# Kernel optimization log

Measured on AMD Instinct MI355X. Metric: run time of the kernel, lower is better.

Reference implementation:

```python
import jax, jax.numpy as jnp
import numpy as np

N_E = 8192
E_DIM = 256
BETA = 0.25


def setup_inputs() -> dict:
    key = jax.random.key(0)
    k1, k2 = jax.random.split(key)
    z = jax.random.normal(k1, (16, E_DIM, 32, 32), dtype=jnp.float32)
    # nn.Embedding init: uniform(-1/n_e, 1/n_e)
    e_w = jax.random.uniform(k2, (N_E, E_DIM), dtype=jnp.float32,
                             minval=-1.0 / N_E, maxval=1.0 / N_E)
    return {"z": z, "e_w": e_w}


def reference(z, e_w):
    B, C, H, W = z.shape  # C == e_dim
    n_e = e_w.shape[0]
    # (B,C,H,W) -> (N, D)
    z_flat = jnp.transpose(z, (0, 2, 3, 1)).reshape(-1, C)
    # squared euclidean distances: ||z||^2 + ||e||^2 - 2 z.e  -> (N, n_e)
    z_sq = jnp.sum(z_flat * z_flat, axis=1, keepdims=True)
    e_sq = jnp.sum(e_w * e_w, axis=1)
    distances = z_sq + e_sq[None, :] - 2.0 * (z_flat @ e_w.T)
    indices = jnp.argmin(distances, axis=1)  # (N,)
    one_hot = jax.nn.one_hot(indices, n_e, dtype=z.dtype)  # (N, n_e)
    # one_hot @ e_w == gather
    z_q_flat = e_w[indices]
    z_q = jnp.transpose(z_q_flat.reshape(B, H, W, C), (0, 3, 1, 2))
    sg = jax.lax.stop_gradient
    loss_embed = jnp.mean((sg(z_q) - z) ** 2)
    loss_commit = jnp.mean((z_q - sg(z)) ** 2)
    loss = loss_embed + BETA * loss_commit
    # straight-through estimator
    z_q_st = z + sg(z_q - z)
    avg_probs = jnp.mean(one_hot, axis=0)
    perplexity = jnp.exp(-jnp.sum(avg_probs * jnp.log(avg_probs + 1e-10)))
    return loss, z_q_st, perplexity, one_hot, indices
```

## Files before the change

kernel.cpp:

```cpp
#include <hip/hip_runtime.h>
#include <hip/hip_bf16.h>
#include <math.h>

#define N_ROWS 16384
#define DIM    256
#define NE     8192
#define QMARGIN 21

#define SOFF 4194308

typedef __bf16 bf16x8 __attribute__((ext_vector_type(8)));
typedef float  f32x4  __attribute__((ext_vector_type(4)));
typedef float  vf4    __attribute__((ext_vector_type(4)));

__device__ __forceinline__ void gload_lds16(const __bf16* g, __bf16* l) {
  __builtin_amdgcn_global_load_lds(
      (const __attribute__((address_space(1))) unsigned int*)g,
      (__attribute__((address_space(3))) unsigned int*)l, 16, 0, 0);
}

__global__ void k_prep(const float* __restrict__ z, float* __restrict__ zf,
                       __bf16* __restrict__ zfb) {
  __shared__ float tile[32][33];
  int ct = blockIdx.x, ht = blockIdx.y, b = blockIdx.z;
  int tx = threadIdx.x & 31, ty = threadIdx.x >> 5;
  int c0 = ct * 32, hw0 = ht * 32;
  const size_t zb = (size_t)b * 256 * 1024;
#pragma unroll
  for (int p = 0; p < 4; ++p) {
    int c = p * 8 + ty;
    tile[c][tx] = z[zb + (size_t)(c0 + c) * 1024 + hw0 + tx];
  }
  __syncthreads();
#pragma unroll
  for (int p = 0; p < 4; ++p) {
    int r = p * 8 + ty;
    zf[(size_t)(b * 1024 + hw0 + r) * DIM + c0 + tx] = tile[tx][r];
  }
  if (threadIdx.x < 128) {
    int r = threadIdx.x >> 2, kc = threadIdx.x & 3;
    int row = b * 1024 + hw0 + r;
    bf16x8 v;
#pragma unroll
    for (int j = 0; j < 8; ++j) v[j] = (__bf16)tile[kc * 8 + j][r];
    int tn = row >> 7, g = (row >> 4) & 7, m15 = row & 15, kt = c0 >> 5;
    *(bf16x8*)(zfb + (size_t)tn * 32768 + kt * 4096 + g * 512 + (kc * 16 + m15) * 8) = v;
  }
}

__global__ void k_cvt_e(const float* __restrict__ ew, __bf16* __restrict__ ewb) {
  int gid = blockIdx.x * 256 + threadIdx.x;
  int r = gid >> 5, kc8 = gid & 31;
  const float* s = ew + (size_t)r * DIM + kc8 * 8;
  float4 v0 = *(const float4*)s, v1 = *(const float4*)(s + 4);
  bf16x8 v = {(__bf16)v0.x, (__bf16)v0.y, (__bf16)v0.z, (__bf16)v0.w,
              (__bf16)v1.x, (__bf16)v1.y, (__bf16)v1.z, (__bf16)v1.w};
  int t = r >> 7, g = (r >> 4) & 7, m15 = r & 15, kt = kc8 >> 2, kc = kc8 & 3;
  *(bf16x8*)(ewb + (size_t)t * 32768 + kt * 4096 + g * 512 + (kc * 16 + m15) * 8) = v;
}

__global__ __launch_bounds__(256, 2) void k_score(const __bf16* __restrict__ zfb,
                                                  const __bf16* __restrict__ ewb,
                                                  int2* __restrict__ part2) {
  __shared__ __align__(16) __bf16 Afull[32768];
  __shared__ __align__(16) __bf16 Bs[2][4096];
  const int tid = threadIdx.x;
  const int lane = tid & 63, wave = tid >> 6;
  const int wm = wave >> 1, wn = wave & 1;
  const int quad = lane >> 4, l15 = lane & 15;
  const int bx = blockIdx.x, byc = blockIdx.y;
  const __bf16* Ag = zfb + (size_t)bx * 32768;
  const __bf16* Bg = ewb + (size_t)byc * 262144;

  {
    const int base = wave * 8192;
#pragma unroll
    for (int i = 0; i < 16; ++i)
      gload_lds16(Ag + base + i * 512 + lane * 8, Afull + base + i * 512);
  }
  {
    const int boff = wave * 1024;
    gload_lds16(Bg + boff + lane * 8, Bs[0] + boff);
    gload_lds16(Bg + boff + 512 + lane * 8, Bs[0] + boff + 512);
  }

  f32x4 acc[4][4];
#pragma unroll
  for (int i = 0; i < 4; ++i)
#pragma unroll
    for (int j = 0; j < 4; ++j) acc[i][j] = (f32x4){0.f, 0.f, 0.f, 0.f};
  int r1[16], r2[16];
#pragma unroll
  for (int i = 0; i < 16; ++i) { r1[i] = 0x7fffffff; r2[i] = 0x7fffffff; }

  for (int it = 0; it < 64; ++it) {
    const int bt = it >> 3, kt = it & 7, buf = it & 1;
    __syncthreads();
    if (it < 63) {
      const int nx = it + 1;
      const __bf16* src = Bg + (nx >> 3) * 32768 + (nx & 7) * 4096 + wave * 1024;
      gload_lds16(src + lane * 8, Bs[buf ^ 1] + wave * 1024);
      gload_lds16(src + 512 + lane * 8, Bs[buf ^ 1] + wave * 1024 + 512);
    }
    bf16x8 af[4], bfr[4];
#pragma unroll
    for (int mi = 0; mi < 4; ++mi)
      af[mi] = *(const bf16x8*)(Afull + kt * 4096 + (wm * 4 + mi) * 512 + lane * 8);
#pragma unroll
    for (int ni = 0; ni < 4; ++ni)
      bfr[ni] = *(const bf16x8*)(Bs[buf] + (wn * 4 + ni) * 512 + lane * 8);
#pragma unroll
    for (int mi = 0; mi < 4; ++mi)
#pragma unroll
      for (int ni = 0; ni < 4; ++ni)
        acc[mi][ni] = __builtin_amdgcn_mfma_f32_16x16x32_bf16(af[mi], bfr[ni],
                                                              acc[mi][ni], 0, 0, 0);
    if (kt == 7) {
      const int colb = byc * 1024 + bt * 128 + wn * 64;
#pragma unroll
      for (int mi = 0; mi < 4; ++mi) {
#pragma unroll
        for (int rg = 0; rg < 4; ++rg) {
          const int idx = mi * 4 + rg;
          float s0 = -2.f * acc[mi][0][rg], s1 = -2.f * acc[mi][1][rg];
          float s2 = -2.f * acc[mi][2][rg], s3 = -2.f * acc[mi][3][rg];
          int q0 = min(max((int)((s0 + 1.0f) * 131072.0f), 0), 262143);
          int q1 = min(max((int)((s1 + 1.0f) * 131072.0f), 0), 262143);
          int q2 = min(max((int)((s2 + 1.0f) * 131072.0f), 0), 262143);
          int q3 = min(max((int)((s3 + 1.0f) * 131072.0f), 0), 262143);
          int k0 = (q0 << 13) | (colb + l15);
          int k1 = (q1 << 13) | (colb + 16 + l15);
          int k2 = (q2 << 13) | (colb + 32 + l15);
          int k3 = (q3 << 13) | (colb + 48 + l15);
          int a = min(k0, k1), bb = max(k0, k1);
          int c = min(k2, k3), dd = max(k2, k3);
          int t1 = min(a, c);
          int t2 = min(max(a, c), min(bb, dd));
          int n1 = min(r1[idx], t1);
          int n2 = min(max(r1[idx], t1), min(r2[idx], t2));
          r1[idx] = n1; r2[idx] = n2;
        }
      }
#pragma unroll
      for (int i = 0; i < 4; ++i)
#pragma unroll
        for (int j = 0; j < 4; ++j) acc[i][j] = (f32x4){0.f, 0.f, 0.f, 0.f};
    }
  }

#pragma unroll
  for (int mi = 0; mi < 4; ++mi) {
#pragma unroll
    for (int rg = 0; rg < 4; ++rg) {
      const int idx = mi * 4 + rg;
      int k1 = r1[idx], k2 = r2[idx];
#pragma unroll
      for (int d = 1; d < 16; d <<= 1) {
        int o1 = __shfl_xor(k1, d), o2 = __shfl_xor(k2, d);
        k2 = min(max(k1, o1), min(k2, o2));
        k1 = min(k1, o1);
      }
      if (l15 == 0) {
        int row = bx * 128 + wm * 64 + mi * 16 + quad * 4 + rg;
        int2 v; v.x = k1; v.y = k2;
        part2[row * 16 + byc * 2 + wn] = v;
      }
    }
  }
}

__device__ __forceinline__ float np_sumsq_128(const float* __restrict__ p) {
  float r[8];
#pragma unroll
  for (int j = 0; j < 8; ++j) r[j] = __fmul_rn(p[j], p[j]);
  for (int i = 8; i < 128; i += 8) {
#pragma unroll
    for (int j = 0; j < 8; ++j) r[j] = __fadd_rn(r[j], __fmul_rn(p[i + j], p[i + j]));
  }
  return __fadd_rn(__fadd_rn(__fadd_rn(r[0], r[1]), __fadd_rn(r[2], r[3])),
                   __fadd_rn(__fadd_rn(r[4], r[5]), __fadd_rn(r[6], r[7])));
}

__global__ __launch_bounds__(256) void k_pick(const int2* __restrict__ part2,
                                              const float* __restrict__ zf,
                                              const float* __restrict__ ew,
                                              float* __restrict__ idxF,
                                              float* __restrict__ losspart) {
  __shared__ int cand[4][40];
  __shared__ int cnts[4];
  const int t = threadIdx.x, lane = t & 63, wv = t >> 6;
  const int row = blockIdx.x * 4 + wv;
  if (lane == 0) cnts[wv] = 0;
  int2 pv;
  if (lane < 16) pv = part2[row * 16 + lane];
  else { pv.x = 0x7fffffff; pv.y = 0x7fffffff; }
  int kmin = pv.x;
#pragma unroll
  for (int d = 1; d < 64; d <<= 1) kmin = min(kmin, __shfl_xor(kmin, d));
  const int qthr = min((kmin >> 13) + QMARGIN, 262143);
  const int kthr = (qthr << 13) | 8191;
  __syncthreads();
  if (lane < 16) {
    if (pv.x <= kthr) { int p = atomicAdd(&cnts[wv], 1); cand[wv][p] = pv.x & 8191; }
    if (pv.y <= kthr) { int p = atomicAdd(&cnts[wv], 1); cand[wv][p] = pv.y & 8191; }
  }
  __syncthreads();
  const int cnt = cnts[wv];
  const float* zr = zf + (size_t)row * DIM;
  float bd = INFINITY; int bj = 0x7fffffff;
  if (lane < cnt) {
    int j = cand[wv][lane];
    const float* e = ew + (size_t)j * DIM;
    float acc = 0.f;
    for (int k = 0; k < DIM; ++k) acc = __builtin_fmaf(zr[k], e[k], acc);
    float esq = __fadd_rn(np_sumsq_128(e), np_sumsq_128(e + 128));
    float zsq = __fadd_rn(np_sumsq_128(zr), np_sumsq_128(zr + 128));
    bd = __fsub_rn(__fadd_rn(zsq, esq), __fmul_rn(2.0f, acc));
    bj = j;
  }
#pragma unroll
  for (int d = 1; d < 64; d <<= 1) {
    float od = __shfl_xor(bd, d); int oj = __shfl_xor(bj, d);
    if (od < bd || (od == bd && oj < bj)) { bd = od; bj = oj; }
  }
  int c = lane * 4;
  float4 e4 = *reinterpret_cast<const float4*>(ew + (size_t)bj * DIM + c);
  float4 z4 = *reinterpret_cast<const float4*>(zr + c);
  float t0 = __fsub_rn(e4.x, z4.x), t1 = __fsub_rn(e4.y, z4.y);
  float t2 = __fsub_rn(e4.z, z4.z), t3 = __fsub_rn(e4.w, z4.w);
  float s = __fadd_rn(__fadd_rn(__fmul_rn(t0, t0), __fmul_rn(t1, t1)),
                      __fadd_rn(__fmul_rn(t2, t2), __fmul_rn(t3, t3)));
#pragma unroll
  for (int d = 1; d < 64; d <<= 1) s += __shfl_xor(s, d);
  if (lane == 0) {
    idxF[row] = (float)bj;
    losspart[row] = s;
  }
}

__global__ __launch_bounds__(256) void k_scalars(const float* __restrict__ idxF,
                                                 const float* __restrict__ losspart,
                                                 float* __restrict__ out) {
  __shared__ int hist[NE];
  __shared__ float red[256];
  int t = threadIdx.x;
  for (int i = t; i < NE; i += 256) hist[i] = 0;
  __syncthreads();
  float ls = 0.f;
  for (int i = t; i < N_ROWS; i += 256) {
    atomicAdd(&hist[(int)idxF[i]], 1);
    ls += losspart[i];
  }
  __syncthreads();
  float es = 0.f;
  for (int i = t; i < NE; i += 256) {
    float p = (float)hist[i] * (1.0f / 16384.0f);
    es += p * logf(p + 1e-10f);
  }
  red[t] = es; __syncthreads();
  for (int w = 128; w > 0; w >>= 1) { if (t < w) red[t] += red[t + w]; __syncthreads(); }
  float esum = red[0]; __syncthreads();
  red[t] = ls; __syncthreads();
  for (int w = 128; w > 0; w >>= 1) { if (t < w) red[t] += red[t + w]; __syncthreads(); }
  if (t == 0) {
    out[4194305] = expf(-esum);
    float m = red[0] * (1.0f / 4194304.0f);
    out[0] = __fadd_rn(m, __fmul_rn(0.25f, m));
  }
}

__global__ void k_zq_out(const float* __restrict__ z, const float* __restrict__ ew,
                         const float* __restrict__ idxF, float* __restrict__ out) {
  __shared__ float tileE[32][33];
  __shared__ int sidx[32];
  int ct = blockIdx.x, ht = blockIdx.y, b = blockIdx.z;
  int tx = threadIdx.x & 31, ty = threadIdx.x >> 5;
  int c0 = ct * 32, hw0 = ht * 32;
  if (threadIdx.x < 32) sidx[threadIdx.x] = (int)idxF[b * 1024 + hw0 + threadIdx.x];
  __syncthreads();
#pragma unroll
  for (int p = 0; p < 4; ++p) {
    int r = p * 8 + ty;
    tileE[tx][r] = ew[(size_t)sidx[r] * DIM + c0 + tx];
  }
  __syncthreads();
  float* outq = out + 1;
#pragma unroll
  for (int p = 0; p < 4; ++p) {
    int cl = p * 8 + ty;
    size_t gi = (size_t)(b * 256 + c0 + cl) * 1024 + hw0 + tx;
    float zv = z[gi];
    outq[gi] = __fadd_rn(zv, __fsub_rn(tileE[cl][tx], zv));
  }
}

__global__ void k_onehot(const float* __restrict__ idxF, float* __restrict__ out) {
  int row = blockIdx.x;
  int t = threadIdx.x;
  int idx = (int)idxF[row];
  float* p = out + 4194306 + (size_t)row * NE;
  if (t == 0) {
    float2 h; h.x = (0 == idx) ? 1.f : 0.f; h.y = (1 == idx) ? 1.f : 0.f;
    *(float2*)p = h;
    float2 q; q.x = (8190 == idx) ? 1.f : 0.f; q.y = (8191 == idx) ? 1.f : 0.f;
    *(float2*)(p + 8190) = q;
  }
  vf4* b4 = (vf4*)(p + 2);
#pragma unroll
  for (int it = 0; it < 8; ++it) {
    int i = it * 256 + t;
    if (i < 2047) {
      int c = 2 + i * 4;
      vf4 v;
      v.x = (c     == idx) ? 1.f : 0.f;
      v.y = (c + 1 == idx) ? 1.f : 0.f;
      v.z = (c + 2 == idx) ? 1.f : 0.f;
      v.w = (c + 3 == idx) ? 1.f : 0.f;
      __builtin_nontemporal_store(v, b4 + i);
    }
  }
}

extern "C" void kernel_launch(void* const* d_in, const int* in_sizes, int n_in,
                              void* d_out, int out_size, void* d_ws, size_t ws_size,
                              hipStream_t stream) {
  const float* z  = (const float*)d_in[0];
  const float* ew = (const float*)d_in[1];
  float* out = (float*)d_out;
  float*  zf    = out + SOFF;
  __bf16* zfb   = (__bf16*)(out + SOFF + 4194304);
  __bf16* ewb   = (__bf16*)(out + SOFF + 6291456);
  int2*   part2 = (int2*)(out + SOFF + 7340032);
  float*  lprt  = out + SOFF + 7864320;
  float*  idxF  = out + 138412034;

  k_prep<<<dim3(8, 32, 16), 256, 0, stream>>>(z, zf, zfb);
  k_cvt_e<<<dim3(1024), 256, 0, stream>>>(ew, ewb);
  k_score<<<dim3(128, 8), 256, 0, stream>>>(zfb, ewb, part2);
  k_pick<<<dim3(4096), 256, 0, stream>>>(part2, zf, ew, idxF, lprt);
  k_scalars<<<1, 256, 0, stream>>>(idxF, lprt, out);
  k_zq_out<<<dim3(8, 32, 16), 256, 0, stream>>>(z, ew, idxF, out);
  k_onehot<<<dim3(16384), 256, 0, stream>>>(idxF, out);
}
```

Before: 925.0 us.

## Overlap one-hot zero-fill with the score GEMM and scatter the ones afterward

```diff
diff --git a/kernel.cpp b/kernel.cpp
--- a/kernel.cpp
+++ b/kernel.cpp
@@ -8,6 +8,11 @@
 #define QMARGIN 21
 
 #define SOFF 4194308
+#define Z_HEAD 12083202ULL
+#define Z4_BASE 12083204ULL
+#define N4_TOTAL 31582207ULL
+#define C4_PER_BLK 30843ULL
+#define Z_TAIL 138412032ULL
 
 typedef __bf16 bf16x8 __attribute__((ext_vector_type(8)));
 typedef float  f32x4  __attribute__((ext_vector_type(4)));
@@ -61,7 +66,8 @@
 
 __global__ __launch_bounds__(256, 2) void k_score(const __bf16* __restrict__ zfb,
                                                   const __bf16* __restrict__ ewb,
-                                                  int2* __restrict__ part2) {
+                                                  int2* __restrict__ part2,
+                                                  float* __restrict__ oz) {
   __shared__ __align__(16) __bf16 Afull[32768];
   __shared__ __align__(16) __bf16 Bs[2][4096];
   const int tid = threadIdx.x;
@@ -69,8 +75,19 @@
   const int wm = wave >> 1, wn = wave & 1;
   const int quad = lane >> 4, l15 = lane & 15;
   const int bx = blockIdx.x, byc = blockIdx.y;
+  const int bid = byc * 128 + bx;
   const __bf16* Ag = zfb + (size_t)bx * 32768;
   const __bf16* Bg = ewb + (size_t)byc * 262144;
+  const size_t blk4 = (size_t)bid * C4_PER_BLK;
+  f32x4* zdst = (f32x4*)(oz + Z4_BASE);
+  const f32x4 zero4 = {0.f, 0.f, 0.f, 0.f};
+
+  if (bid == 0 && tid == 0) {
+    __builtin_nontemporal_store(0.f, oz + Z_HEAD);
+    __builtin_nontemporal_store(0.f, oz + Z_HEAD + 1);
+    __builtin_nontemporal_store(0.f, oz + Z_TAIL);
+    __builtin_nontemporal_store(0.f, oz + Z_TAIL + 1);
+  }
 
   {
     const int base = wave * 8192;
@@ -101,6 +118,16 @@
       const __bf16* src = Bg + (nx >> 3) * 32768 + (nx & 7) * 4096 + wave * 1024;
       gload_lds16(src + lane * 8, Bs[buf ^ 1] + wave * 1024);
       gload_lds16(src + 512 + lane * 8, Bs[buf ^ 1] + wave * 1024 + 512);
+    }
+    if (it <= 60) {
+#pragma unroll
+      for (int s = 0; s < 2; ++s) {
+        size_t slot = (size_t)(it * 2 + s) * 256 + tid;
+        if (slot < C4_PER_BLK) {
+          size_t g4 = blk4 + slot;
+          if (g4 < N4_TOTAL) __builtin_nontemporal_store(zero4, zdst + g4);
+        }
+      }
     }
     bf16x8 af[4], bfr[4];
 #pragma unroll
@@ -295,28 +322,37 @@
 }
 
 __global__ void k_onehot(const float* __restrict__ idxF, float* __restrict__ out) {
-  int row = blockIdx.x;
+  int bx = blockIdx.x;
   int t = threadIdx.x;
-  int idx = (int)idxF[row];
-  float* p = out + 4194306 + (size_t)row * NE;
-  if (t == 0) {
-    float2 h; h.x = (0 == idx) ? 1.f : 0.f; h.y = (1 == idx) ? 1.f : 0.f;
-    *(float2*)p = h;
-    float2 q; q.x = (8190 == idx) ? 1.f : 0.f; q.y = (8191 == idx) ? 1.f : 0.f;
-    *(float2*)(p + 8190) = q;
-  }
-  vf4* b4 = (vf4*)(p + 2);
-#pragma unroll
-  for (int it = 0; it < 8; ++it) {
-    int i = it * 256 + t;
-    if (i < 2047) {
-      int c = 2 + i * 4;
-      vf4 v;
-      v.x = (c     == idx) ? 1.f : 0.f;
-      v.y = (c + 1 == idx) ? 1.f : 0.f;
-      v.z = (c + 2 == idx) ? 1.f : 0.f;
-      v.w = (c + 3 == idx) ? 1.f : 0.f;
-      __builtin_nontemporal_store(v, b4 + i);
+  if (bx < 963) {
+    int row = bx;
+    int idx = (int)idxF[row];
+    float* p = out + 4194306 + (size_t)row * NE;
+    if (t == 0) {
+      float2 h; h.x = (0 == idx) ? 1.f : 0.f; h.y = (1 == idx) ? 1.f : 0.f;
+      *(float2*)p = h;
+      float2 q; q.x = (8190 == idx) ? 1.f : 0.f; q.y = (8191 == idx) ? 1.f : 0.f;
+      *(float2*)(p + 8190) = q;
+    }
+    vf4* b4 = (vf4*)(p + 2);
+#pragma unroll
+    for (int it = 0; it < 8; ++it) {
+      int i = it * 256 + t;
+      if (i < 2047) {
+        int c = 2 + i * 4;
+        vf4 v;
+        v.x = (c     == idx) ? 1.f : 0.f;
+        v.y = (c + 1 == idx) ? 1.f : 0.f;
+        v.z = (c + 2 == idx) ? 1.f : 0.f;
+        v.w = (c + 3 == idx) ? 1.f : 0.f;
+        __builtin_nontemporal_store(v, b4 + i);
+      }
+    }
+  } else {
+    int row = 963 + (bx - 963) * 256 + t;
+    if (row < N_ROWS) {
+      int idx = (int)idxF[row];
+      out[4194306 + (size_t)row * NE + idx] = 1.0f;
     }
   }
 }
@@ -336,9 +372,9 @@
 
   k_prep<<<dim3(8, 32, 16), 256, 0, stream>>>(z, zf, zfb);
   k_cvt_e<<<dim3(1024), 256, 0, stream>>>(ew, ewb);
-  k_score<<<dim3(128, 8), 256, 0, stream>>>(zfb, ewb, part2);
+  k_score<<<dim3(128, 8), 256, 0, stream>>>(zfb, ewb, part2, out);
   k_pick<<<dim3(4096), 256, 0, stream>>>(part2, zf, ew, idxF, lprt);
   k_scalars<<<1, 256, 0, stream>>>(idxF, lprt, out);
   k_zq_out<<<dim3(8, 32, 16), 256, 0, stream>>>(z, ew, idxF, out);
-  k_onehot<<<dim3(16384), 256, 0, stream>>>(idxF, out);
-}
+  k_onehot<<<dim3(1024), 256, 0, stream>>>(idxF, out);
+}
```

New measurement: 828.8 us. 10.4% less time.
